# Optimization experiments

Hardware: AMD Instinct MI355X
Metric: run time of the kernel (lower is better)

Reference implementation:

```python
import jax, jax.numpy as jnp
import numpy as np

B, N, D, V, Y = 4, 4096, 512, 50257, 16000

def setup_inputs() -> dict:
    key = jax.random.key(0)
    ks = jax.random.split(key, 5)
    # token ids in [1, V): avoid pad_id=0 so no attention row is fully -inf
    M_s = jax.random.randint(ks[0], (B, N), 1, V)
    E_v = jax.random.normal(ks[1], (V, D), jnp.float32) * 0.02
    E_y = jax.random.normal(ks[2], (Y, D), jnp.float32) * 0.02
    s = 1.0 / np.sqrt(D)  # kaiming_uniform(a=sqrt(5)) bound for [D,D]
    W_A = jax.random.uniform(ks[3], (D, D), jnp.float32, minval=-s, maxval=s)
    W_O = jax.random.uniform(ks[4], (D, D), jnp.float32, minval=-s, maxval=s)
    gamma = jnp.ones((D,), jnp.float32)
    beta = jnp.zeros((D,), jnp.float32)
    return {"M_s": M_s, "E_v": E_v, "E_y": E_y, "W_A": W_A, "W_O": W_O,
            "gamma": gamma, "beta": beta}

def _layer_norm(x, g, b, eps=1e-5):
    mu = jnp.mean(x, axis=-1, keepdims=True)
    var = jnp.mean(jnp.square(x - mu), axis=-1, keepdims=True)
    return (x - mu) * jax.lax.rsqrt(var + eps) * g + b

def reference(M_s, E_v, E_y, W_A, W_O, gamma, beta):
    # Self-attention branch (v_q=None), dropout in eval mode (identity).
    X = E_v[M_s]                                   # [B, N, D]
    mask = (M_s != 0)                              # [B, N] padding mask
    # logits = (X @ W_A) @ X^T
    logits = jnp.einsum('bnd,de,bme->bnm', X, W_A, X)   # [B, N, N]
    logits = jnp.where(mask[:, None, :], logits, -jnp.inf)
    # positional + causal bias: D = -|i-j| with future (i<j) set to -inf
    i = jnp.arange(N, dtype=jnp.float32)[:, None]
    j = jnp.arange(N, dtype=jnp.float32)[None, :]
    dist = i - j
    bias = jnp.where(dist >= 0, -dist, -jnp.inf)        # [N, N]
    A = jax.nn.softmax(logits + bias, axis=-1)          # [B, N, N]
    Q_c = jnp.einsum('bnm,bmd,de->bne', A, X, W_O)      # [B, N, D]
    H = _layer_norm(Q_c + X, gamma, beta)               # [B, N, D]
    y_logits = jnp.einsum('bnd,yd->bny', H, E_y)        # [B, N, Y]
    return y_logits, A
```

## Files before the change

kernel.cpp:

```cpp
#include <hip/hip_runtime.h>


#define DEVINL __device__ __forceinline__

typedef __attribute__((ext_vector_type(8))) short bf16x8;
typedef __attribute__((ext_vector_type(4))) float f32x4;
typedef unsigned short u16;

#define BB 4
#define NN 4096
#define DD 512
#define YY 16000
#define YPAD 16128
#define ROWS (BB * NN)

DEVINL u16 f2bf(float x) {
  unsigned u = __float_as_uint(x);
  return (u16)((u + 0x7fffu + ((u >> 16) & 1u)) >> 16);
}

DEVINL float bf2f(u16 h) { return __uint_as_float((unsigned)h << 16); }

DEVINL void gload16(const void* g, void* l) {
  __builtin_amdgcn_global_load_lds(
      (const __attribute__((address_space(1))) void*)g,
      (__attribute__((address_space(3))) void*)l, 16, 0, 0);
}

DEVINL void zero_acc(f32x4 acc[4][4]) {
#pragma unroll
  for (int m = 0; m < 4; ++m)
#pragma unroll
    for (int n = 0; n < 4; ++n) {
      acc[m][n][0] = 0.f; acc[m][n][1] = 0.f;
      acc[m][n][2] = 0.f; acc[m][n][3] = 0.f;
    }
}

DEVINL void gemm_bt_core(const u16* __restrict__ A, int lda,
                         const u16* __restrict__ Bm, int ldb, int ksteps,
                         u16* sA, u16* sB, f32x4 acc[4][4], int tid) {
  const int lane = tid & 63, w = tid >> 6;
  const int wr = (w >> 1) * 64, wc = (w & 1) * 64;
  const int c0 = w * 128 + lane, c1 = c0 + 64;
  const u16* gA0 = A + (size_t)(c0 >> 2) * lda + (c0 & 3) * 8;
  const u16* gA1 = A + (size_t)(c1 >> 2) * lda + (c1 & 3) * 8;
  const u16* gB0 = Bm + (size_t)(c0 >> 2) * ldb + (c0 & 3) * 8;
  const u16* gB1 = Bm + (size_t)(c1 >> 2) * ldb + (c1 & 3) * 8;
  u16* lA0 = sA + w * 1024;  u16* lA1 = lA0 + 512;
  u16* lB0 = sB + w * 1024;  u16* lB1 = lB0 + 512;
  const int fr = lane & 15, fk = (lane >> 4) * 8;

  for (int kt = 0; kt < ksteps; ++kt) {
    __syncthreads();
    gload16(gA0 + kt * 32, lA0);
    gload16(gA1 + kt * 32, lA1);
    gload16(gB0 + kt * 32, lB0);
    gload16(gB1 + kt * 32, lB1);
    __syncthreads();
    bf16x8 af[4], bfv[4];
#pragma unroll
    for (int m = 0; m < 4; ++m)
      af[m] = *(const bf16x8*)(sA + (wr + m * 16 + fr) * 32 + fk);
#pragma unroll
    for (int n = 0; n < 4; ++n)
      bfv[n] = *(const bf16x8*)(sB + (wc + n * 16 + fr) * 32 + fk);
#pragma unroll
    for (int m = 0; m < 4; ++m)
#pragma unroll
      for (int n = 0; n < 4; ++n)
        acc[m][n] = __builtin_amdgcn_mfma_f32_16x16x32_bf16(af[m], bfv[n],
                                                            acc[m][n], 0, 0, 0);
  }
}

#define C256_STAGE(kt, buf)                                    \
  {                                                            \
    const u16* a0 = Ag + (kt) * 64;                            \
    const u16* b0 = Bg + (kt) * 64;                            \
    u16* Lb = lds + (buf) * 32768;                             \
    gload16(a0 + offE0, Lb + d0);                              \
    gload16(a0 + offE1, Lb + d1);                              \
    gload16(a0 + 65536 + offE0, Lb + 8192 + d0);               \
    gload16(a0 + 65536 + offE1, Lb + 8192 + d1);               \
    gload16(b0 + offE0, Lb + 16384 + d0);                      \
    gload16(b0 + offE1, Lb + 16384 + d1);                      \
    gload16(b0 + 65536 + offE0, Lb + 24576 + d0);              \
    gload16(b0 + 65536 + offE1, Lb + 24576 + d1);              \
  }

DEVINL void core256(const u16* __restrict__ Ag, const u16* __restrict__ Bg,
                    u16* lds, f32x4 (&acc)[8][4], int tid) {
  const int lane = tid & 63, w = tid >> 6;
  const int wm = w >> 2, wn = w & 3;

  int offE0, offE1;
  {
    int q = tid;
    int r = (((q >> 6) >> 1) << 4) | ((q >> 2) & 15);
    int c = (((q >> 6) & 1) << 5) |
            (((q & 3) << 3) ^ (((q >> 5) & 1) << 4) ^ (((q >> 4) & 1) << 3));
    offE0 = r * DD + c;
    q = 512 + tid;
    r = (((q >> 6) >> 1) << 4) | ((q >> 2) & 15);
    c = (((q >> 6) & 1) << 5) |
        (((q & 3) << 3) ^ (((q >> 5) & 1) << 4) ^ (((q >> 4) & 1) << 3));
    offE1 = r * DD + c;
  }
  const int d0 = w * 512, d1 = 4096 + w * 512;

  int x = (lane & 15) * 64 + ((lane >> 4) & 3) * 16;
  int fxu = (x ^ (((x >> 9) & 1) << 5) ^ (((x >> 8) & 1) << 4)) >> 1;

#pragma unroll
  for (int m = 0; m < 8; ++m)
#pragma unroll
    for (int n = 0; n < 4; ++n) {
      acc[m][n][0] = 0.f; acc[m][n][1] = 0.f;
      acc[m][n][2] = 0.f; acc[m][n][3] = 0.f;
    }

  C256_STAGE(0, 0);
  C256_STAGE(1, 1);
  asm volatile("s_waitcnt vmcnt(8)" ::: "memory");
  __syncthreads();

  for (int c = 0; c < 8; ++c) {
    const u16* L = lds + (c & 1) * 32768;
    const u16* pa = L + wm * 8192;
    const u16* pb = L + 16384 + (wn >> 1) * 8192 + (wn & 1) * 4096;
    bf16x8 af[4][2], bf[4][2];
#pragma unroll
    for (int n = 0; n < 2; ++n)
#pragma unroll
      for (int ks = 0; ks < 2; ++ks)
        bf[n][ks] = *(const bf16x8*)(pb + (n * 2 + ks) * 512 + fxu);
#pragma unroll
    for (int m = 0; m < 4; ++m)
#pragma unroll
      for (int ks = 0; ks < 2; ++ks)
        af[m][ks] = *(const bf16x8*)(pa + (m * 2 + ks) * 512 + fxu);
    __builtin_amdgcn_s_setprio(1);
#pragma unroll
    for (int m = 0; m < 4; ++m)
#pragma unroll
      for (int n = 0; n < 2; ++n)
#pragma unroll
        for (int ks = 0; ks < 2; ++ks)
          acc[m][n] = __builtin_amdgcn_mfma_f32_16x16x32_bf16(
              af[m][ks], bf[n][ks], acc[m][n], 0, 0, 0);
    __builtin_amdgcn_s_setprio(0);
#pragma unroll
    for (int n = 2; n < 4; ++n)
#pragma unroll
      for (int ks = 0; ks < 2; ++ks)
        bf[n][ks] = *(const bf16x8*)(pb + (n * 2 + ks) * 512 + fxu);
    __builtin_amdgcn_s_setprio(1);
#pragma unroll
    for (int m = 0; m < 4; ++m)
#pragma unroll
      for (int n = 2; n < 4; ++n)
#pragma unroll
        for (int ks = 0; ks < 2; ++ks)
          acc[m][n] = __builtin_amdgcn_mfma_f32_16x16x32_bf16(
              af[m][ks], bf[n][ks], acc[m][n], 0, 0, 0);
    __builtin_amdgcn_s_setprio(0);
#pragma unroll
    for (int m = 0; m < 4; ++m)
#pragma unroll
      for (int ks = 0; ks < 2; ++ks)
        af[m][ks] = *(const bf16x8*)(pa + ((m + 4) * 2 + ks) * 512 + fxu);
    __builtin_amdgcn_s_setprio(1);
#pragma unroll
    for (int m = 0; m < 4; ++m)
#pragma unroll
      for (int n = 0; n < 2; ++n)
#pragma unroll
        for (int ks = 0; ks < 2; ++ks)
          acc[m + 4][n] = __builtin_amdgcn_mfma_f32_16x16x32_bf16(
              af[m][ks], bf[n][ks], acc[m + 4][n], 0, 0, 0);
#pragma unroll
    for (int m = 0; m < 4; ++m)
#pragma unroll
      for (int n = 2; n < 4; ++n)
#pragma unroll
        for (int ks = 0; ks < 2; ++ks)
          acc[m + 4][n] = __builtin_amdgcn_mfma_f32_16x16x32_bf16(
              af[m][ks], bf[n][ks], acc[m + 4][n], 0, 0, 0);
    __builtin_amdgcn_s_setprio(0);

    __syncthreads();
    if (c < 6) {
      C256_STAGE(c + 2, c & 1);
      asm volatile("s_waitcnt vmcnt(8)" ::: "memory");
    } else if (c == 6) {
      asm volatile("s_waitcnt vmcnt(0)" ::: "memory");
    }
    __syncthreads();
  }
}

__global__ __launch_bounds__(256) void prep_all(const int* __restrict__ Ms,
                                                const float* __restrict__ Ev,
                                                const float* __restrict__ WA,
                                                const float* __restrict__ WO,
                                                const float* __restrict__ Ey,
                                                u16* __restrict__ Xb,
                                                u16* __restrict__ WAt,
                                                u16* __restrict__ WOt,
                                                u16* __restrict__ Eyb) {
  __shared__ u16 t[64][65];
  int bx = blockIdx.x, tid = threadIdx.x;
  if (bx < 8192) {
    int row = bx * 2 + (tid >> 7);
    int t4 = tid & 127;
    int tok = Ms[row];
    float4 v = *(const float4*)(Ev + (size_t)tok * DD + t4 * 4);
    *(ushort4*)(Xb + (size_t)row * DD + t4 * 4) =
        make_ushort4(f2bf(v.x), f2bf(v.y), f2bf(v.z), f2bf(v.w));
  } else if (bx < 8320) {
    int k = bx - 8192;
    const float* W = (k < 64) ? WA : WO;
    u16* Wt = (k < 64) ? WAt : WOt;
    k &= 63;
    int dt = k >> 3, et = k & 7;
#pragma unroll
    for (int p = 0; p < 16; ++p) {
      int e = tid + 256 * p; int r = e >> 6, c = e & 63;
      t[r][c] = f2bf(W[(size_t)(dt * 64 + r) * DD + et * 64 + c]);
    }
    __syncthreads();
#pragma unroll
    for (int p = 0; p < 16; ++p) {
      int e = tid + 256 * p; int r = e >> 6, c = e & 63;
      Wt[(size_t)(et * 64 + r) * DD + dt * 64 + c] = t[c][r];
    }
  } else {
    size_t i4 = (size_t)(bx - 8320) * 256 + tid;
    size_t row = i4 >> 7;
    ushort4 h;
    if (row < YY) {
      float4 v = *(const float4*)(Ey + i4 * 4);
      h = make_ushort4(f2bf(v.x), f2bf(v.y), f2bf(v.z), f2bf(v.w));
    } else {
      h = make_ushort4(0, 0, 0, 0);
    }
    *(ushort4*)(Eyb + i4 * 4) = h;
  }
}

__global__ __launch_bounds__(256) void prep_xt(const u16* __restrict__ Xb,
                                               u16* __restrict__ XbT) {
  __shared__ u16 t[64][65];
  int tid = threadIdx.x;
  int nt = blockIdx.x, dt = blockIdx.y, b = blockIdx.z;
  const u16* src = Xb + ((size_t)b * NN + nt * 64) * DD + dt * 64;
#pragma unroll
  for (int p = 0; p < 16; ++p) {
    int e = tid + 256 * p; int r = e >> 6, c = e & 63;
    t[r][c] = src[(size_t)r * DD + c];
  }
  __syncthreads();
  u16* dst = XbT + ((size_t)b * DD + dt * 64) * NN + nt * 64;
#pragma unroll
  for (int p = 0; p < 16; ++p) {
    int e = tid + 256 * p; int r = e >> 6, c = e & 63;
    dst[(size_t)r * NN + c] = t[c][r];
  }
}

__global__ __launch_bounds__(256) void k2_xw(const u16* __restrict__ Xb,
                                             const u16* __restrict__ WAt,
                                             u16* __restrict__ XWb) {
  __shared__ u16 sA[4096], sB[4096];
  f32x4 acc[4][4]; zero_acc(acc);
  int tid = threadIdx.x;
  size_t row0 = (size_t)blockIdx.x * 128, col0 = (size_t)blockIdx.y * 128;
  gemm_bt_core(Xb + row0 * DD, DD, WAt + col0 * DD, DD, DD / 32, sA, sB, acc, tid);
  int lane = tid & 63, w = tid >> 6;
  int wr = (w >> 1) * 64, wc = (w & 1) * 64;
  int cr = (lane >> 4) * 4, cc = lane & 15;
#pragma unroll
  for (int m = 0; m < 4; ++m)
#pragma unroll
    for (int n = 0; n < 4; ++n)
#pragma unroll
      for (int r = 0; r < 4; ++r) {
        size_t gi = row0 + wr + m * 16 + cr + r;
        size_t gj = col0 + wc + n * 16 + cc;
        XWb[gi * DD + gj] = f2bf(acc[m][n][r]);
      }
}

__global__ __launch_bounds__(256) void k3_scores(const u16* __restrict__ XWb,
                                                 const u16* __restrict__ Xb,
                                                 u16* __restrict__ Ebf) {
  int t = blockIdx.x, b = blockIdx.z;
  int ib = (int)((sqrtf(8.f * (float)t + 1.f) - 1.f) * 0.5f);
  while ((ib + 1) * (ib + 2) / 2 <= t) ++ib;
  while (ib * (ib + 1) / 2 > t) --ib;
  int jb = t - ib * (ib + 1) / 2;
  __shared__ u16 sA[4096], sB[4096];
  f32x4 acc[4][4]; zero_acc(acc);
  int tid = threadIdx.x;
  const u16* Ap = XWb + ((size_t)b * NN + ib * 128) * DD;
  const u16* Bp = Xb  + ((size_t)b * NN + jb * 128) * DD;
  gemm_bt_core(Ap, DD, Bp, DD, DD / 32, sA, sB, acc, tid);
  int lane = tid & 63, w = tid >> 6;
  int wr = (w >> 1) * 64, wc = (w & 1) * 64;
  int cr = (lane >> 4) * 4, cc = lane & 15;
  u16* Eb = Ebf + (size_t)b * NN * NN;
#pragma unroll
  for (int m = 0; m < 4; ++m)
#pragma unroll
    for (int n = 0; n < 4; ++n)
#pragma unroll
      for (int r = 0; r < 4; ++r) {
        int i = ib * 128 + wr + m * 16 + cr + r;
        int j = jb * 128 + wc + n * 16 + cc;
        float e = (j > i) ? 0.f : __expf(acc[m][n][r] - (float)(i - j));
        Eb[(size_t)i * NN + j] = f2bf(e);
      }
}

__global__ __launch_bounds__(256) void k5_ax(const u16* __restrict__ Ebf,
                                             const u16* __restrict__ XbT,
                                             u16* __restrict__ AXb) {
  int u = blockIdx.x;
  int half = u >> 8, v = u & 255;
  int ib = v & 31; if (half) ib = 31 - ib;
  int db = (v >> 5) & 3;
  int b = (half << 1) | (v >> 7);
  __shared__ u16 sA[4096], sB[4096];
  f32x4 acc[4][4]; zero_acc(acc);
  int tid = threadIdx.x;
  const u16* Ap = Ebf + ((size_t)b * NN + ib * 128) * NN;
  const u16* Bp = XbT + ((size_t)b * DD + db * 128) * NN;
  gemm_bt_core(Ap, NN, Bp, NN, (ib + 1) * 4, sA, sB, acc, tid);
  int lane = tid & 63, w = tid >> 6;
  int wr = (w >> 1) * 64, wc = (w & 1) * 64;
  int cr = (lane >> 4) * 4, cc = lane & 15;
#pragma unroll
  for (int m = 0; m < 4; ++m)
#pragma unroll
    for (int n = 0; n < 4; ++n)
#pragma unroll
      for (int r = 0; r < 4; ++r) {
        int i = ib * 128 + wr + m * 16 + cr + r;
        int d = db * 128 + wc + n * 16 + cc;
        AXb[((size_t)b * NN + i) * DD + d] = f2bf(acc[m][n][r]);
      }
}

__global__ __launch_bounds__(256) void k6_qc(const u16* __restrict__ AXb,
                                             const u16* __restrict__ WOt,
                                             u16* __restrict__ Qcb) {
  __shared__ u16 sA[4096], sB[4096];
  f32x4 acc[4][4]; zero_acc(acc);
  int tid = threadIdx.x;
  size_t row0 = (size_t)blockIdx.x * 128, col0 = (size_t)blockIdx.y * 128;
  gemm_bt_core(AXb + row0 * DD, DD, WOt + col0 * DD, DD, DD / 32, sA, sB, acc, tid);
  int lane = tid & 63, w = tid >> 6;
  int wr = (w >> 1) * 64, wc = (w & 1) * 64;
  int cr = (lane >> 4) * 4, cc = lane & 15;
#pragma unroll
  for (int m = 0; m < 4; ++m)
#pragma unroll
    for (int n = 0; n < 4; ++n)
#pragma unroll
      for (int r = 0; r < 4; ++r) {
        size_t gi = row0 + wr + m * 16 + cr + r;
        size_t gj = col0 + wc + n * 16 + cc;
        Qcb[gi * DD + gj] = f2bf(acc[m][n][r]);
      }
}

__global__ __launch_bounds__(256) void k4_softmax(const u16* __restrict__ Ebf,
                                                  float* __restrict__ Aout,
                                                  float* __restrict__ invb) {
  __shared__ u16 srow[NN];
  __shared__ float red[4];
  size_t row = blockIdx.x;
  int i = (int)(row & (NN - 1));
  const u16* E = Ebf + row * (size_t)NN;
  float* S = Aout + row * (size_t)NN;
  int len = i + 1, tid = threadIdx.x;
  int padend = (len + 127) & ~127;
  int nc = padend >> 3;
  for (int v = tid; v < nc; v += 256)
    *(uint4*)(srow + v * 8) = *(const uint4*)(E + v * 8);
  __syncthreads();
  float l = 0.f;
  for (int v = tid; v < nc; v += 256) {
    uint4 x = *(const uint4*)(srow + v * 8);
    l += bf2f((u16)(x.x & 0xffff)) + bf2f((u16)(x.x >> 16));
    l += bf2f((u16)(x.y & 0xffff)) + bf2f((u16)(x.y >> 16));
    l += bf2f((u16)(x.z & 0xffff)) + bf2f((u16)(x.z >> 16));
    l += bf2f((u16)(x.w & 0xffff)) + bf2f((u16)(x.w >> 16));
  }
#pragma unroll
  for (int o = 32; o; o >>= 1) l += __shfl_xor(l, o);
  if ((tid & 63) == 0) red[tid >> 6] = l;
  __syncthreads();
  float inv = 1.f / (red[0] + red[1] + red[2] + red[3]);
  if (tid == 0) invb[row] = inv;
  for (int v = tid; v < NN / 4; v += 256) {
    int k = v * 4;
    float4 a = make_float4(0.f, 0.f, 0.f, 0.f);
    if (k < padend) {
      ushort4 e = *(const ushort4*)(srow + k);
      a = make_float4(bf2f(e.x) * inv, bf2f(e.y) * inv,
                      bf2f(e.z) * inv, bf2f(e.w) * inv);
    }
    *(float4*)(S + k) = a;
  }
}

__global__ __launch_bounds__(128) void k6b_ln(const u16* __restrict__ Qcb,
                                              const u16* __restrict__ Xb,
                                              const float* __restrict__ invb,
                                              const float* __restrict__ gamma,
                                              const float* __restrict__ beta,
                                              u16* __restrict__ Hb) {
  int row = blockIdx.x, tid = threadIdx.x;
  float inv = invb[row];
  ushort4 qu = *(const ushort4*)(Qcb + (size_t)row * DD + tid * 4);
  ushort4 xu = *(const ushort4*)(Xb + (size_t)row * DD + tid * 4);
  float v0 = bf2f(qu.x) * inv + bf2f(xu.x), v1 = bf2f(qu.y) * inv + bf2f(xu.y);
  float v2 = bf2f(qu.z) * inv + bf2f(xu.z), v3 = bf2f(qu.w) * inv + bf2f(xu.w);
  float s = v0 + v1 + v2 + v3;
  float s2 = v0 * v0 + v1 * v1 + v2 * v2 + v3 * v3;
#pragma unroll
  for (int o = 32; o; o >>= 1) { s += __shfl_xor(s, o); s2 += __shfl_xor(s2, o); }
  __shared__ float r1[2], r2[2];
  int lane = tid & 63, w = tid >> 6;
  if (lane == 0) { r1[w] = s; r2[w] = s2; }
  __syncthreads();
  s = r1[0] + r1[1]; s2 = r2[0] + r2[1];
  float mu = s * (1.f / 512.f);
  float var = s2 * (1.f / 512.f) - mu * mu;
  float rs = 1.f / sqrtf(var + 1e-5f);
  float4 g  = *(const float4*)(gamma + tid * 4);
  float4 be = *(const float4*)(beta + tid * 4);
  ushort4 h = make_ushort4(f2bf((v0 - mu) * rs * g.x + be.x),
                           f2bf((v1 - mu) * rs * g.y + be.y),
                           f2bf((v2 - mu) * rs * g.z + be.z),
                           f2bf((v3 - mu) * rs * g.w + be.w));
  *(ushort4*)(Hb + (size_t)row * DD + tid * 4) = h;
}

__global__ __launch_bounds__(512, 2) void k7_logits(const u16* __restrict__ Hb,
                                                    const u16* __restrict__ Eyb,
                                                    float* __restrict__ Yout) {
  __shared__ u16 lds[65536];
  const int tid = threadIdx.x;
  const int lane = tid & 63, w = tid >> 6;
  const int wm = w >> 2, wn = w & 3;

  int id = blockIdx.x;
  int swz = (id & 7) * (4032 / 8) + (id >> 3);
  size_t row0 = (size_t)(swz & 63) * 256;
  size_t col0 = (size_t)(swz >> 6) * 256;

  f32x4 acc[8][4];
  core256(Hb + row0 * DD, Eyb + col0 * DD, lds, acc, tid);

  const int cr = (lane >> 4) * 4, cc = lane & 15;
#pragma unroll
  for (int m = 0; m < 8; ++m)
#pragma unroll
    for (int n = 0; n < 4; ++n) {
      size_t gj = col0 + wn * 64 + n * 16 + cc;
      if (gj < YY) {
        size_t gi = row0 + wm * 128 + m * 16 + cr;
#pragma unroll
        for (int rr = 0; rr < 4; ++rr)
          Yout[(gi + rr) * (size_t)YY + gj] = acc[m][n][rr];
      }
    }
}

extern "C" void kernel_launch(void* const* d_in, const int* in_sizes, int n_in,
                              void* d_out, int out_size, void* d_ws, size_t ws_size,
                              hipStream_t stream) {
  (void)in_sizes; (void)n_in; (void)out_size; (void)ws_size;
  const int*   Ms    = (const int*)d_in[0];
  const float* Ev    = (const float*)d_in[1];
  const float* Ey    = (const float*)d_in[2];
  const float* WA    = (const float*)d_in[3];
  const float* WO    = (const float*)d_in[4];
  const float* gamma = (const float*)d_in[5];
  const float* beta  = (const float*)d_in[6];

  float* Yout = (float*)d_out;
  float* Aout = Yout + (size_t)BB * NN * YY;

  char* w = (char*)d_ws;
  u16* Xb  = (u16*)w; w += (size_t)ROWS * DD * 2;
  u16* XbT = (u16*)w; w += (size_t)BB * DD * NN * 2;
  u16* XWb = (u16*)w; w += (size_t)ROWS * DD * 2;
  u16* AXb = (u16*)w; w += (size_t)ROWS * DD * 2;
  u16* Hb  = (u16*)w; w += (size_t)ROWS * DD * 2;
  u16* WAt = (u16*)w; w += (size_t)DD * DD * 2;
  u16* WOt = (u16*)w; w += (size_t)DD * DD * 2;
  u16* Eyb = (u16*)w; w += (size_t)YPAD * DD * 2;
  u16* Ebf = (u16*)w; w += (size_t)ROWS * NN * 2;
  float* invb = (float*)w; w += (size_t)ROWS * 4;
  u16* Qcb = XWb;

  prep_all<<<16384, 256, 0, stream>>>(Ms, Ev, WA, WO, Ey, Xb, WAt, WOt, Eyb);
  prep_xt<<<dim3(NN / 64, DD / 64, BB), 256, 0, stream>>>(Xb, XbT);
  k2_xw<<<dim3(ROWS / 128, DD / 128), 256, 0, stream>>>(Xb, WAt, XWb);
  k3_scores<<<dim3(528, 1, BB), 256, 0, stream>>>(XWb, Xb, Ebf);
  k5_ax<<<512, 256, 0, stream>>>(Ebf, XbT, AXb);
  k6_qc<<<dim3(ROWS / 128, DD / 128), 256, 0, stream>>>(AXb, WOt, Qcb);
  k4_softmax<<<ROWS, 256, 0, stream>>>(Ebf, Aout, invb);
  k6b_ln<<<ROWS, 128, 0, stream>>>(Qcb, Xb, invb, gamma, beta, Hb);
  k7_logits<<<dim3(64 * 63), 512, 0, stream>>>(Hb, Eyb, Yout);
}
```

Baseline: 820.5 us.

## Reassociate W_O into X before attention and transpose logits GEMM for vector stores

Computes (X·W_O)^T directly with a new GEMM kernel, which replaces the X transpose kernel and the separate Qc GEMM after the attention-weighted sum. Attention then multiplies E by X·W_O and writes Qc directly, removing one kernel launch and the AX round trip through memory. The final logits GEMM swaps operand roles so each lane stores a contiguous float4 along Y instead of scalar stores. The transposed-output GEMM writes with a strided pattern, and the reassociation changes where bf16 rounding happens.

New measurement: 865.4 us. 1.05x slower.

```diff
diff --git a/kernel.cpp b/kernel.cpp
--- a/kernel.cpp
+++ b/kernel.cpp
@@ -249,26 +249,6 @@
   }
 }
 
-__global__ __launch_bounds__(256) void prep_xt(const u16* __restrict__ Xb,
-                                               u16* __restrict__ XbT) {
-  __shared__ u16 t[64][65];
-  int tid = threadIdx.x;
-  int nt = blockIdx.x, dt = blockIdx.y, b = blockIdx.z;
-  const u16* src = Xb + ((size_t)b * NN + nt * 64) * DD + dt * 64;
-#pragma unroll
-  for (int p = 0; p < 16; ++p) {
-    int e = tid + 256 * p; int r = e >> 6, c = e & 63;
-    t[r][c] = src[(size_t)r * DD + c];
-  }
-  __syncthreads();
-  u16* dst = XbT + ((size_t)b * DD + dt * 64) * NN + nt * 64;
-#pragma unroll
-  for (int p = 0; p < 16; ++p) {
-    int e = tid + 256 * p; int r = e >> 6, c = e & 63;
-    dst[(size_t)r * NN + c] = t[c][r];
-  }
-}
-
 __global__ __launch_bounds__(256) void k2_xw(const u16* __restrict__ Xb,
                                              const u16* __restrict__ WAt,
                                              u16* __restrict__ XWb) {
@@ -289,6 +269,31 @@
         size_t gi = row0 + wr + m * 16 + cr + r;
         size_t gj = col0 + wc + n * 16 + cc;
         XWb[gi * DD + gj] = f2bf(acc[m][n][r]);
+      }
+}
+
+__global__ __launch_bounds__(256) void k_wot(const u16* __restrict__ WOt,
+                                             const u16* __restrict__ Xb,
+                                             u16* __restrict__ XWoT) {
+  __shared__ u16 sA[4096], sB[4096];
+  f32x4 acc[4][4]; zero_acc(acc);
+  int tid = threadIdx.x;
+  int et = blockIdx.x, it = blockIdx.y, b = blockIdx.z;
+  const u16* Ap = WOt + (size_t)et * 128 * DD;
+  const u16* Bp = Xb + ((size_t)b * NN + it * 128) * DD;
+  gemm_bt_core(Ap, DD, Bp, DD, DD / 32, sA, sB, acc, tid);
+  int lane = tid & 63, w = tid >> 6;
+  int wr = (w >> 1) * 64, wc = (w & 1) * 64;
+  int cr = (lane >> 4) * 4, cc = lane & 15;
+#pragma unroll
+  for (int m = 0; m < 4; ++m)
+#pragma unroll
+    for (int n = 0; n < 4; ++n)
+#pragma unroll
+      for (int r = 0; r < 4; ++r) {
+        size_t e = (size_t)et * 128 + wr + m * 16 + cr + r;
+        size_t i = (size_t)it * 128 + wc + n * 16 + cc;
+        XWoT[((size_t)b * DD + e) * NN + i] = f2bf(acc[m][n][r]);
       }
 }
 
@@ -324,8 +329,8 @@
 }
 
 __global__ __launch_bounds__(256) void k5_ax(const u16* __restrict__ Ebf,
-                                             const u16* __restrict__ XbT,
-                                             u16* __restrict__ AXb) {
+                                             const u16* __restrict__ XWoT,
+                                             u16* __restrict__ Qcb) {
   int u = blockIdx.x;
   int half = u >> 8, v = u & 255;
   int ib = v & 31; if (half) ib = 31 - ib;
@@ -335,7 +340,7 @@
   f32x4 acc[4][4]; zero_acc(acc);
   int tid = threadIdx.x;
   const u16* Ap = Ebf + ((size_t)b * NN + ib * 128) * NN;
-  const u16* Bp = XbT + ((size_t)b * DD + db * 128) * NN;
+  const u16* Bp = XWoT + ((size_t)b * DD + db * 128) * NN;
   gemm_bt_core(Ap, NN, Bp, NN, (ib + 1) * 4, sA, sB, acc, tid);
   int lane = tid & 63, w = tid >> 6;
   int wr = (w >> 1) * 64, wc = (w & 1) * 64;
@@ -348,30 +353,7 @@
       for (int r = 0; r < 4; ++r) {
         int i = ib * 128 + wr + m * 16 + cr + r;
         int d = db * 128 + wc + n * 16 + cc;
-        AXb[((size_t)b * NN + i) * DD + d] = f2bf(acc[m][n][r]);
-      }
-}
-
-__global__ __launch_bounds__(256) void k6_qc(const u16* __restrict__ AXb,
-                                             const u16* __restrict__ WOt,
-                                             u16* __restrict__ Qcb) {
-  __shared__ u16 sA[4096], sB[4096];
-  f32x4 acc[4][4]; zero_acc(acc);
-  int tid = threadIdx.x;
-  size_t row0 = (size_t)blockIdx.x * 128, col0 = (size_t)blockIdx.y * 128;
-  gemm_bt_core(AXb + row0 * DD, DD, WOt + col0 * DD, DD, DD / 32, sA, sB, acc, tid);
-  int lane = tid & 63, w = tid >> 6;
-  int wr = (w >> 1) * 64, wc = (w & 1) * 64;
-  int cr = (lane >> 4) * 4, cc = lane & 15;
-#pragma unroll
-  for (int m = 0; m < 4; ++m)
-#pragma unroll
-    for (int n = 0; n < 4; ++n)
-#pragma unroll
-      for (int r = 0; r < 4; ++r) {
-        size_t gi = row0 + wr + m * 16 + cr + r;
-        size_t gj = col0 + wc + n * 16 + cc;
-        Qcb[gi * DD + gj] = f2bf(acc[m][n][r]);
+        Qcb[((size_t)b * NN + i) * DD + d] = f2bf(acc[m][n][r]);
       }
 }
 
@@ -463,21 +445,20 @@
   size_t col0 = (size_t)(swz >> 6) * 256;
 
   f32x4 acc[8][4];
-  core256(Hb + row0 * DD, Eyb + col0 * DD, lds, acc, tid);
+  core256(Eyb + col0 * DD, Hb + row0 * DD, lds, acc, tid);
 
   const int cr = (lane >> 4) * 4, cc = lane & 15;
 #pragma unroll
-  for (int m = 0; m < 8; ++m)
-#pragma unroll
-    for (int n = 0; n < 4; ++n) {
-      size_t gj = col0 + wn * 64 + n * 16 + cc;
-      if (gj < YY) {
-        size_t gi = row0 + wm * 128 + m * 16 + cr;
-#pragma unroll
-        for (int rr = 0; rr < 4; ++rr)
-          Yout[(gi + rr) * (size_t)YY + gj] = acc[m][n][rr];
+  for (int m = 0; m < 8; ++m) {
+    size_t p0 = col0 + wm * 128 + m * 16 + cr;
+    if (p0 < YY) {
+#pragma unroll
+      for (int n = 0; n < 4; ++n) {
+        size_t q = row0 + wn * 64 + n * 16 + cc;
+        *(f32x4*)(Yout + q * (size_t)YY + p0) = acc[m][n];
       }
     }
+  }
 }
 
 extern "C" void kernel_launch(void* const* d_in, const int* in_sizes, int n_in,
@@ -496,24 +477,22 @@
   float* Aout = Yout + (size_t)BB * NN * YY;
 
   char* w = (char*)d_ws;
-  u16* Xb  = (u16*)w; w += (size_t)ROWS * DD * 2;
-  u16* XbT = (u16*)w; w += (size_t)BB * DD * NN * 2;
-  u16* XWb = (u16*)w; w += (size_t)ROWS * DD * 2;
-  u16* AXb = (u16*)w; w += (size_t)ROWS * DD * 2;
-  u16* Hb  = (u16*)w; w += (size_t)ROWS * DD * 2;
-  u16* WAt = (u16*)w; w += (size_t)DD * DD * 2;
-  u16* WOt = (u16*)w; w += (size_t)DD * DD * 2;
-  u16* Eyb = (u16*)w; w += (size_t)YPAD * DD * 2;
-  u16* Ebf = (u16*)w; w += (size_t)ROWS * NN * 2;
+  u16* Xb   = (u16*)w; w += (size_t)ROWS * DD * 2;
+  u16* XWoT = (u16*)w; w += (size_t)BB * DD * NN * 2;
+  u16* XWb  = (u16*)w; w += (size_t)ROWS * DD * 2;
+  u16* Hb   = (u16*)w; w += (size_t)ROWS * DD * 2;
+  u16* WAt  = (u16*)w; w += (size_t)DD * DD * 2;
+  u16* WOt  = (u16*)w; w += (size_t)DD * DD * 2;
+  u16* Eyb  = (u16*)w; w += (size_t)YPAD * DD * 2;
+  u16* Ebf  = (u16*)w; w += (size_t)ROWS * NN * 2;
   float* invb = (float*)w; w += (size_t)ROWS * 4;
   u16* Qcb = XWb;
 
   prep_all<<<16384, 256, 0, stream>>>(Ms, Ev, WA, WO, Ey, Xb, WAt, WOt, Eyb);
-  prep_xt<<<dim3(NN / 64, DD / 64, BB), 256, 0, stream>>>(Xb, XbT);
+  k_wot<<<dim3(DD / 128, NN / 128, BB), 256, 0, stream>>>(WOt, Xb, XWoT);
   k2_xw<<<dim3(ROWS / 128, DD / 128), 256, 0, stream>>>(Xb, WAt, XWb);
   k3_scores<<<dim3(528, 1, BB), 256, 0, stream>>>(XWb, Xb, Ebf);
-  k5_ax<<<512, 256, 0, stream>>>(Ebf, XbT, AXb);
-  k6_qc<<<dim3(ROWS / 128, DD / 128), 256, 0, stream>>>(AXb, WOt, Qcb);
+  k5_ax<<<512, 256, 0, stream>>>(Ebf, XWoT, Qcb);
   k4_softmax<<<ROWS, 256, 0, stream>>>(Ebf, Aout, invb);
   k6b_ln<<<ROWS, 128, 0, stream>>>(Qcb, Xb, invb, gamma, beta, Hb);
   k7_logits<<<dim3(64 * 63), 512, 0, stream>>>(Hb, Eyb, Yout);
```
